# Performance work log

Measured on AMD Instinct MI355X. Metric: run time of the kernel, lower is better.

## Reference

```python
import jax, jax.numpy as jnp
import numpy as np

N, E = 50000, 800000
IN, HID, OUT, H = 128, 32, 32, 4
NEG_SLOPE = 0.2
EPS = 1e-5


def layernorm(x, g, b):
    mu = x.mean(-1, keepdims=True)
    var = ((x - mu) ** 2).mean(-1, keepdims=True)
    return (x - mu) * jax.lax.rsqrt(var + EPS) * g + b


def gat_conv(x, src, dst, W, a_s, a_d, bias, heads, ch, concat):
    n = x.shape[0]
    h = (x @ W).reshape(n, heads, ch)               # [N,H,C]
    alpha_s = (h * a_s).sum(-1)                     # [N,H]
    alpha_d = (h * a_d).sum(-1)                     # [N,H]
    e = jax.nn.leaky_relu(alpha_s[src] + alpha_d[dst], NEG_SLOPE)  # [E,H]
    m = jax.ops.segment_max(e, dst, num_segments=n)
    m = jnp.where(jnp.isfinite(m), m, 0.0)
    ex = jnp.exp(e - m[dst])
    denom = jax.ops.segment_sum(ex, dst, num_segments=n)
    alpha = ex / (denom[dst] + 1e-16)               # [E,H]
    msg = h[src] * alpha[:, :, None]                # [E,H,C]
    out = jax.ops.segment_sum(msg, dst, num_segments=n)  # [N,H,C]
    out = out.reshape(n, heads * ch) if concat else out.mean(axis=1)
    return out + bias


def setup_inputs() -> dict:
    key = jax.random.key(0)
    ks = jax.random.split(key, 24)
    HC = HID * H
    s = 0.05
    inp = {
        "x": jax.random.normal(ks[0], (N, IN), jnp.float32),
        "edge_index": jax.random.randint(ks[1], (2, E), 0, N),
        "W1": jax.random.normal(ks[2], (IN, HC), jnp.float32) * s,
        "as1": jax.random.normal(ks[3], (H, HID), jnp.float32) * s,
        "ad1": jax.random.normal(ks[4], (H, HID), jnp.float32) * s,
        "b1": jnp.zeros((HC,), jnp.float32),
        "g1": jnp.ones((HC,), jnp.float32),
        "be1": jnp.zeros((HC,), jnp.float32),
        "W2": jax.random.normal(ks[5], (HC, HC), jnp.float32) * s,
        "as2": jax.random.normal(ks[6], (H, HID), jnp.float32) * s,
        "ad2": jax.random.normal(ks[7], (H, HID), jnp.float32) * s,
        "b2": jnp.zeros((HC,), jnp.float32),
        "g2": jnp.ones((HC,), jnp.float32),
        "be2": jnp.zeros((HC,), jnp.float32),
        "W3": jax.random.normal(ks[8], (HC, OUT * H), jnp.float32) * s,
        "as3": jax.random.normal(ks[9], (H, OUT), jnp.float32) * s,
        "ad3": jax.random.normal(ks[10], (H, OUT), jnp.float32) * s,
        "b3": jnp.zeros((OUT,), jnp.float32),
        "Wsk": jax.random.normal(ks[11], (IN, HC), jnp.float32) * s,
        "bsk": jnp.zeros((HC,), jnp.float32),
    }
    return inp


def reference(x, edge_index, W1, as1, ad1, b1, g1, be1, W2, as2, ad2, b2, g2, be2, W3, as3, ad3, b3, Wsk, bsk):
    n = x.shape[0]
    loops = jnp.arange(n, dtype=edge_index.dtype)
    src = jnp.concatenate([edge_index[0], loops])
    dst = jnp.concatenate([edge_index[1], loops])
    h = gat_conv(x, src, dst, W1, as1, ad1, b1, H, HID, True)
    h = jax.nn.elu(h)
    h = layernorm(h, g1, be1)
    h = h + (x @ Wsk + bsk)  # residual (dropout is identity in eval)
    h = gat_conv(h, src, dst, W2, as2, ad2, b2, H, HID, True)
    h = jax.nn.elu(h)
    h = layernorm(h, g2, be2)
    h = gat_conv(h, src, dst, W3, as3, ad3, b3, H, OUT, False)
    return h
```

## Files before the change

### kernel.cpp

```cpp
#include <hip/hip_runtime.h>
#include <hip/hip_bf16.h>

typedef __attribute__((ext_vector_type(8))) short short8;
typedef __attribute__((ext_vector_type(4))) float f32x4;
using bf16 = __hip_bfloat16;

#define NEG_SLOPE 0.2f
#define LN_EPS 1e-5f
#define SCAT_EPB 4096

__device__ __forceinline__ unsigned short f2bfu(float v) {
    bf16 t = __float2bfloat16(v);
    unsigned short s;
    __builtin_memcpy(&s, &t, 2);
    return s;
}
__device__ __forceinline__ short f2bf(float v) {
    bf16 t = __float2bfloat16(v);
    short s;
    __builtin_memcpy(&s, &t, 2);
    return s;
}
__device__ __forceinline__ unsigned packbf(float a, float b) {
    return (unsigned)f2bfu(a) | ((unsigned)f2bfu(b) << 16);
}
__device__ __forceinline__ float bflo(unsigned u) { return __uint_as_float(u << 16); }
__device__ __forceinline__ float bfhi(unsigned u) { return __uint_as_float(u & 0xffff0000u); }
__device__ __forceinline__ float bf1(unsigned short u) { return __uint_as_float(((unsigned)u) << 16); }

__device__ __forceinline__ int computeFlag(const void* x) {
    const uint4* u4 = (const uint4*)x;
    int lane = threadIdx.x & 63;
    float m = 0.f;
    for (int i = lane; i < 1024; i += 64) {
        uint4 q = u4[i];
        unsigned vv[4] = {q.x, q.y, q.z, q.w};
#pragma unroll
        for (int k = 0; k < 4; ++k) {
            float a = fabsf(bflo(vv[k]));
            float b = fabsf(bfhi(vv[k]));
            m = fmaxf(m, (a == a) ? a : 1e30f);
            m = fmaxf(m, (b == b) ? b : 1e30f);
        }
    }
    for (int d = 1; d < 64; d <<= 1) m = fmaxf(m, __shfl_xor(m, d));
    return (m > 1e4f) ? 1 : 0;
}

struct Ptr4 { const void* p[4]; };
struct Ptr14 { const void* p[14]; };
struct Ptr3 { const void* p[3]; };
struct Ptr6 { const void* p[6]; };
__global__ void stage_k(const void* __restrict__ x,
                        Ptr4 Ws, bf16* __restrict__ WT,
                        Ptr14 ptrs, bf16* __restrict__ sv,
                        Ptr3 Wv, Ptr6 av, bf16* __restrict__ vaT,
                        int* __restrict__ dtFlag, int* __restrict__ bucketCur,
                        int CAP) {
    int b = blockIdx.x;
    int f = computeFlag(x);
    if (b < 256) {
        int gid = b * 256 + threadIdx.x;
        int m = gid >> 14;
        int idx = gid & 16383;
        int i = idx >> 7, j = idx & 127;
        const void* W = Ws.p[m];
        float v = f ? ((const float*)W)[idx]
                    : __bfloat162float(((const bf16*)W)[idx]);
        WT[m * 16384 + j * 128 + i] = __float2bfloat16(v);
    } else if (b == 256) {
        for (int i = threadIdx.x; i < 512; i += 256) bucketCur[i] = i * CAP;
        if (threadIdx.x == 0) dtFlag[0] = f;
        for (int k = threadIdx.x; k < 14 * 128; k += 256) {
            int t = k >> 7, i = k & 127;
            int n = (t == 12) ? 32 : 128;
            if (i < n) {
                const void* s = ptrs.p[t];
                float v = f ? ((const float*)s)[i]
                            : __bfloat162float(((const bf16*)s)[i]);
                sv[k] = __float2bfloat16(v);
            }
        }
    } else {
        int gid = (b - 257) * 256 + threadIdx.x;
        int l = gid >> 11;
        if (l >= 3) return;
        int c = (gid >> 7) & 15, k = gid & 127;
        float acc = 0.f;
        if (c < 8) {
            int hd = c & 3;
            const void* W = Wv.p[l];
            const void* a = av.p[l * 2 + (c >> 2)];
            for (int j = 0; j < 32; ++j) {
                float wv = f ? ((const float*)W)[k * 128 + hd * 32 + j]
                             : __bfloat162float(((const bf16*)W)[k * 128 + hd * 32 + j]);
                float avv = f ? ((const float*)a)[hd * 32 + j]
                              : __bfloat162float(((const bf16*)a)[hd * 32 + j]);
                acc += wv * avv;
            }
        }
        vaT[gid] = __float2bfloat16(acc);
    }
}

__global__ __launch_bounds__(256) void mega1_k(
        const void* __restrict__ A, const bf16* __restrict__ WT,
        bf16* __restrict__ out0, bf16* __restrict__ out1,
        const bf16* __restrict__ bias1, const bf16* __restrict__ vaT,
        float* __restrict__ asN, float* __restrict__ adN,
        int N, const int* __restrict__ flag, int gb,
        const int* __restrict__ src, const int* __restrict__ dst,
        int* bucketCur, int* __restrict__ ebuf, int E, int NB, int CAP) {
    __shared__ int lcnt[512], lbase[512];
    if ((int)blockIdx.x >= gb) {
        int t = threadIdx.x;
        int e0 = ((int)blockIdx.x - gb) * SCAT_EPB;
        int cnt = E - e0;
        if (cnt > SCAT_EPB) cnt = SCAT_EPB;
        for (int i = t; i < NB; i += 256) lcnt[i] = 0;
        __syncthreads();
        for (int i = t; i < cnt; i += 256)
            atomicAdd(&lcnt[dst[e0 + i] >> 7], 1);
        __syncthreads();
        for (int i = t; i < NB; i += 256) {
            int c = lcnt[i];
            lbase[i] = c ? atomicAdd(&bucketCur[i], c) : 0;
            lcnt[i] = 0;
        }
        __syncthreads();
        for (int i = t; i < cnt; i += 256) {
            int d = dst[e0 + i];
            int b = d >> 7;
            int pos = lbase[b] + atomicAdd(&lcnt[b], 1);
            if (pos < (b + 1) * CAP)
                ebuf[pos] = ((d & 127) << 16) | src[e0 + i];
        }
        return;
    }
    int wave = threadIdx.x >> 6, lane = threadIdx.x & 63;
    int lm = lane & 15, lk = lane >> 4;
    const short* Ws = (const short*)WT;
    const short* Vs = (const short*)vaT;
    bool f32m = flag[0] != 0;

    short8 bw0[2][4], bw1[2][4];
#pragma unroll
    for (int ct = 0; ct < 2; ++ct) {
        int c = (wave * 2 + ct) * 16 + lm;
#pragma unroll
        for (int kk = 0; kk < 4; ++kk) {
            bw0[ct][kk] = *(const short8*)(Ws + (size_t)c * 128 + kk * 32 + lk * 8);
            bw1[ct][kk] = *(const short8*)(Ws + 16384 + (size_t)c * 128 + kk * 32 + lk * 8);
        }
    }
    short8 va8[4];
    if (wave == 0) {
#pragma unroll
        for (int kk = 0; kk < 4; ++kk)
            va8[kk] = *(const short8*)(Vs + (size_t)lm * 128 + kk * 32 + lk * 8);
    }
    float bv[2][4];
#pragma unroll
    for (int ct = 0; ct < 2; ++ct) {
        int c0 = (wave * 2 + ct) * 16 + lk * 4;
#pragma unroll
        for (int i = 0; i < 4; ++i)
            bv[ct][i] = __bfloat162float(bias1[c0 + i]);
    }

    int stride = gb * 32;
    for (int rowBase = blockIdx.x * 32; rowBase < N; rowBase += stride) {
        short8 af[2][4];
#pragma unroll
        for (int rt = 0; rt < 2; ++rt) {
            int r = rowBase + rt * 16 + lm;
            if (r >= N) r = N - 1;
            if (f32m) {
#pragma unroll
                for (int kk = 0; kk < 4; ++kk) {
                    const float* Af = (const float*)A + (size_t)r * 128 + kk * 32 + lk * 8;
                    float4 q0 = *(const float4*)(Af);
                    float4 q1 = *(const float4*)(Af + 4);
                    short8 v;
                    v[0] = f2bf(q0.x); v[1] = f2bf(q0.y); v[2] = f2bf(q0.z); v[3] = f2bf(q0.w);
                    v[4] = f2bf(q1.x); v[5] = f2bf(q1.y); v[6] = f2bf(q1.z); v[7] = f2bf(q1.w);
                    af[rt][kk] = v;
                }
            } else {
#pragma unroll
                for (int kk = 0; kk < 4; ++kk)
                    af[rt][kk] = *(const short8*)((const short*)A + (size_t)r * 128 + kk * 32 + lk * 8);
            }
        }

        f32x4 acc0[2][2], acc1[2][2];
#pragma unroll
        for (int ct = 0; ct < 2; ++ct)
#pragma unroll
            for (int rt = 0; rt < 2; ++rt) {
                acc0[ct][rt] = (f32x4){0.f, 0.f, 0.f, 0.f};
                acc1[ct][rt] = (f32x4){0.f, 0.f, 0.f, 0.f};
            }
#pragma unroll
        for (int rt = 0; rt < 2; ++rt) {
#pragma unroll
            for (int kk = 0; kk < 4; ++kk) {
                acc0[0][rt] = __builtin_amdgcn_mfma_f32_16x16x32_bf16(bw0[0][kk], af[rt][kk], acc0[0][rt], 0, 0, 0);
                acc0[1][rt] = __builtin_amdgcn_mfma_f32_16x16x32_bf16(bw0[1][kk], af[rt][kk], acc0[1][rt], 0, 0, 0);
                acc1[0][rt] = __builtin_amdgcn_mfma_f32_16x16x32_bf16(bw1[0][kk], af[rt][kk], acc1[0][rt], 0, 0, 0);
                acc1[1][rt] = __builtin_amdgcn_mfma_f32_16x16x32_bf16(bw1[1][kk], af[rt][kk], acc1[1][rt], 0, 0, 0);
            }
        }
#pragma unroll
        for (int ct = 0; ct < 2; ++ct) {
            int c0 = (wave * 2 + ct) * 16 + lk * 4;
#pragma unroll
            for (int rt = 0; rt < 2; ++rt) {
                int r = rowBase + rt * 16 + lm;
                if (r < N) {
                    uint2 pk0, pk1;
                    pk0.x = packbf(acc0[ct][rt][0], acc0[ct][rt][1]);
                    pk0.y = packbf(acc0[ct][rt][2], acc0[ct][rt][3]);
                    pk1.x = packbf(acc1[ct][rt][0] + bv[ct][0], acc1[ct][rt][1] + bv[ct][1]);
                    pk1.y = packbf(acc1[ct][rt][2] + bv[ct][2], acc1[ct][rt][3] + bv[ct][3]);
                    *(uint2*)((unsigned short*)out0 + (size_t)r * 128 + c0) = pk0;
                    *(uint2*)((unsigned short*)out1 + (size_t)r * 128 + c0) = pk1;
                }
            }
        }
        if (wave == 0) {
            f32x4 accA[2];
#pragma unroll
            for (int rt = 0; rt < 2; ++rt) accA[rt] = (f32x4){0.f, 0.f, 0.f, 0.f};
#pragma unroll
            for (int rt = 0; rt < 2; ++rt)
#pragma unroll
                for (int kk = 0; kk < 4; ++kk)
                    accA[rt] = __builtin_amdgcn_mfma_f32_16x16x32_bf16(va8[kk], af[rt][kk], accA[rt], 0, 0, 0);
            if (lk < 2) {
                float* dp = lk ? adN : asN;
#pragma unroll
                for (int rt = 0; rt < 2; ++rt) {
                    int r = rowBase + rt * 16 + lm;
                    if (r < N) *(f32x4*)(dp + (size_t)r * 4) = accA[rt];
                }
            }
        }
    }
}

__global__ __launch_bounds__(256) void build_k(const int* __restrict__ ebuf,
                                               const int* __restrict__ bucketCur,
                                               int* __restrict__ rowSE,
                                               int* __restrict__ colSrc,
                                               int N, int CAP) {
    int b = blockIdx.x, t = threadIdx.x;
    int base = b * CAP;
    int cnt = bucketCur[b] - base;
    if (cnt > CAP) cnt = CAP;
    __shared__ int nodeCnt[128], nodeCur[128], ws2[2];
    if (t < 128) nodeCnt[t] = 0;
    __syncthreads();
    for (int i = t; i < cnt; i += 256)
        atomicAdd(&nodeCnt[ebuf[base + i] >> 16], 1);
    __syncthreads();
    int v = 0, incl = 0;
    if (t < 128) {
        v = nodeCnt[t];
        incl = v;
        for (int d = 1; d < 64; d <<= 1) {
            int u = __shfl_up(incl, d);
            if ((t & 63) >= d) incl += u;
        }
        if ((t & 63) == 63) ws2[t >> 6] = incl;
    }
    __syncthreads();
    if (t < 128) {
        int excl = incl - v + ((t >= 64) ? ws2[0] : 0);
        int node = b * 128 + t;
        if (node < N) {
            rowSE[node * 2] = base + excl;
            rowSE[node * 2 + 1] = base + excl + v;
        }
        nodeCur[t] = excl;
    }
    __syncthreads();
    for (int i = t; i < cnt; i += 256) {
        int p = ebuf[base + i];
        int pos = base + atomicAdd(&nodeCur[p >> 16], 1);
        colSrc[pos] = (p & 0xffff) << 8;
    }
}

__global__ __launch_bounds__(256) void gemm_k(const void* __restrict__ A,
                                              const bf16* __restrict__ WT,
                                              bf16* __restrict__ out0,
                                              const bf16* __restrict__ vaT,
                                              float* __restrict__ asN,
                                              float* __restrict__ adN,
                                              int N) {
    int wave = threadIdx.x >> 6, lane = threadIdx.x & 63;
    int lm = lane & 15, lk = lane >> 4;
    const short* Ws = (const short*)WT;
    const short* Vs = (const short*)vaT;

    short8 bw0[2][4];
#pragma unroll
    for (int ct = 0; ct < 2; ++ct) {
        int c = (wave * 2 + ct) * 16 + lm;
#pragma unroll
        for (int kk = 0; kk < 4; ++kk)
            bw0[ct][kk] = *(const short8*)(Ws + (size_t)c * 128 + kk * 32 + lk * 8);
    }
    short8 va8[4];
    if (wave == 0) {
#pragma unroll
        for (int kk = 0; kk < 4; ++kk)
            va8[kk] = *(const short8*)(Vs + (size_t)lm * 128 + kk * 32 + lk * 8);
    }

    int stride = gridDim.x * 32;
    for (int rowBase = blockIdx.x * 32; rowBase < N; rowBase += stride) {
        short8 af[2][4];
#pragma unroll
        for (int rt = 0; rt < 2; ++rt) {
            int r = rowBase + rt * 16 + lm;
            if (r >= N) r = N - 1;
#pragma unroll
            for (int kk = 0; kk < 4; ++kk)
                af[rt][kk] = *(const short8*)((const short*)A + (size_t)r * 128 + kk * 32 + lk * 8);
        }

        f32x4 acc0[2][2];
#pragma unroll
        for (int ct = 0; ct < 2; ++ct)
#pragma unroll
            for (int rt = 0; rt < 2; ++rt) acc0[ct][rt] = (f32x4){0.f, 0.f, 0.f, 0.f};
#pragma unroll
        for (int rt = 0; rt < 2; ++rt) {
#pragma unroll
            for (int kk = 0; kk < 4; ++kk) {
                acc0[0][rt] = __builtin_amdgcn_mfma_f32_16x16x32_bf16(bw0[0][kk], af[rt][kk], acc0[0][rt], 0, 0, 0);
                acc0[1][rt] = __builtin_amdgcn_mfma_f32_16x16x32_bf16(bw0[1][kk], af[rt][kk], acc0[1][rt], 0, 0, 0);
            }
        }
#pragma unroll
        for (int ct = 0; ct < 2; ++ct) {
            int c0 = (wave * 2 + ct) * 16 + lk * 4;
#pragma unroll
            for (int rt = 0; rt < 2; ++rt) {
                int r = rowBase + rt * 16 + lm;
                if (r < N) {
                    uint2 pk;
                    pk.x = packbf(acc0[ct][rt][0], acc0[ct][rt][1]);
                    pk.y = packbf(acc0[ct][rt][2], acc0[ct][rt][3]);
                    *(uint2*)((unsigned short*)out0 + (size_t)r * 128 + c0) = pk;
                }
            }
        }
        if (wave == 0) {
            f32x4 accA[2];
#pragma unroll
            for (int rt = 0; rt < 2; ++rt) accA[rt] = (f32x4){0.f, 0.f, 0.f, 0.f};
#pragma unroll
            for (int rt = 0; rt < 2; ++rt)
#pragma unroll
                for (int kk = 0; kk < 4; ++kk)
                    accA[rt] = __builtin_amdgcn_mfma_f32_16x16x32_bf16(va8[kk], af[rt][kk], accA[rt], 0, 0, 0);
            if (lk < 2) {
                float* dp = lk ? adN : asN;
#pragma unroll
                for (int rt = 0; rt < 2; ++rt) {
                    int r = rowBase + rt * 16 + lm;
                    if (r < N) *(f32x4*)(dp + (size_t)r * 4) = accA[rt];
                }
            }
        }
    }
}

template <int MODE>
__global__ __launch_bounds__(256) void agg_k(const bf16* __restrict__ h,
                                             const float* __restrict__ asN,
                                             const float* __restrict__ adN,
                                             const int* __restrict__ rowSE,
                                             const int* __restrict__ colSrc,
                                             const bf16* __restrict__ bvec,
                                             const bf16* __restrict__ g,
                                             const bf16* __restrict__ be,
                                             void* outv, int N,
                                             const int* __restrict__ flag) {
    int wv = threadIdx.x >> 6, lane = threadIdx.x & 63;
    int grp = lane >> 4, t = lane & 15;
    int hd = t >> 2;
    const char* hbase = (const char*)h + t * 16;
    const char* abase = (const char*)asN + hd * 4;
    int f = (MODE == 3 && flag) ? flag[0] : 0;
    int nstride = gridDim.x * 4;

    for (int n = blockIdx.x * 4 + wv; n < N; n += nstride) {
        int2 se = ((const int2*)rowSE)[n];
        int st = se.x, en = se.y;
        if (en < st) en = st;

        float adn = adN[(size_t)n * 4 + hd];
        float asn_self = asN[(size_t)n * 4 + hd];
        unsigned hs = *(const unsigned*)((const char*)h + (size_t)n * 256 + t * 16 + grp * 4);

        float a[8];
#pragma unroll
        for (int k = 0; k < 8; ++k) a[k] = 0.f;
        float den = 0.f;

        int j = st + grp;
        int o0 = (j      < en) ? colSrc[j]      : 0;
        int o1 = (j + 4  < en) ? colSrc[j + 4]  : 0;
        int o2 = (j + 8  < en) ? colSrc[j + 8]  : 0;
        int o3 = (j + 12 < en) ? colSrc[j + 12] : 0;
        float av0 = *(const float*)(abase + (o0 >> 4));
        uint4 hq0 = *(const uint4*)(hbase + o0);
        float av1 = *(const float*)(abase + (o1 >> 4));
        uint4 hq1 = *(const uint4*)(hbase + o1);
        float av2 = *(const float*)(abase + (o2 >> 4));
        uint4 hq2 = *(const uint4*)(hbase + o2);
        for (; j < en; j += 4) {
            int o4 = (j + 16 < en) ? colSrc[j + 16] : 0;
            float av3 = *(const float*)(abase + (o3 >> 4));
            uint4 hq3 = *(const uint4*)(hbase + o3);
            float e = av0 + adn;
            float w = __expf(fmaxf(e, NEG_SLOPE * e));
            den += w;
            a[0] += w * bflo(hq0.x); a[1] += w * bfhi(hq0.x);
            a[2] += w * bflo(hq0.y); a[3] += w * bfhi(hq0.y);
            a[4] += w * bflo(hq0.z); a[5] += w * bfhi(hq0.z);
            a[6] += w * bflo(hq0.w); a[7] += w * bfhi(hq0.w);
            o3 = o4;
            av0 = av1; hq0 = hq1;
            av1 = av2; hq1 = hq2;
            av2 = av3; hq2 = hq3;
        }

#pragma unroll
        for (int k = 0; k < 8; ++k) {
            a[k] += __shfl_xor(a[k], 16);
            a[k] += __shfl_xor(a[k], 32);
        }
        den += __shfl_xor(den, 16);
        den += __shfl_xor(den, 32);

        float es = asn_self + adn;
        float wsf = __expf(fmaxf(es, NEG_SLOPE * es));
        den += wsf;

        float s0 = (grp & 1) ? a[2] : a[0];
        float s1 = (grp & 1) ? a[3] : a[1];
        float s2 = (grp & 1) ? a[6] : a[4];
        float s3 = (grp & 1) ? a[7] : a[5];
        float p0 = (grp & 2) ? s2 : s0;
        float p1 = (grp & 2) ? s3 : s1;

        p0 += wsf * bflo(hs);
        p1 += wsf * bfhi(hs);

        float inv = 1.f / (den + 1e-16f);
        float y0 = p0 * inv, y1 = p1 * inv;

        if (MODE == 3) {
            y0 += __shfl_xor(y0, 4); y0 += __shfl_xor(y0, 8); y0 *= 0.25f;
            y1 += __shfl_xor(y1, 4); y1 += __shfl_xor(y1, 8); y1 *= 0.25f;
            if (t < 4) {
                int oc = t * 8 + grp * 2;
                unsigned bp = *(const unsigned*)((const char*)bvec + oc * 2);
                float v0 = y0 + bflo(bp), v1 = y1 + bfhi(bp);
                if (f) {
                    *(float2*)((float*)outv + (size_t)n * 32 + oc) = make_float2(v0, v1);
                } else {
                    ((unsigned*)outv)[(size_t)n * 16 + (oc >> 1)] = packbf(v0, v1);
                }
            }
        } else {
            unsigned short* out = (unsigned short*)outv;
            int boff = t * 16 + grp * 4;
            unsigned bp = *(const unsigned*)((const char*)bvec + boff);
            y0 += bflo(bp); y1 += bfhi(bp);
            y0 = y0 > 0.f ? y0 : (__expf(y0) - 1.f);
            y1 = y1 > 0.f ? y1 : (__expf(y1) - 1.f);
            float s = y0 + y1, q = y0 * y0 + y1 * y1;
#pragma unroll
            for (int d = 1; d < 64; d <<= 1) {
                s += __shfl_xor(s, d);
                q += __shfl_xor(q, d);
            }
            float mu = s * (1.f / 128.f);
            float var = q * (1.f / 128.f) - mu * mu;
            var = fmaxf(var, 0.f);
            float rs = rsqrtf(var + LN_EPS);
            unsigned gp = *(const unsigned*)((const char*)g + boff);
            unsigned ep = *(const unsigned*)((const char*)be + boff);
            float z0 = (y0 - mu) * rs * bflo(gp) + bflo(ep);
            float z1 = (y1 - mu) * rs * bfhi(gp) + bfhi(ep);
            char* op = (char*)out + (size_t)n * 256 + boff;
            if (MODE == 1) {
                unsigned sk = *(const unsigned*)op;
                z0 += bflo(sk); z1 += bfhi(sk);
            }
            *(unsigned*)op = packbf(z0, z1);
        }
    }
}

extern "C" void kernel_launch(void* const* d_in, const int* in_sizes, int n_in,
                              void* d_out, int out_size, void* d_ws, size_t ws_size,
                              hipStream_t stream) {
    const void* x  = d_in[0];
    const int*  ei = (const int*)d_in[1];

    int N = in_sizes[0] / 128;
    int E = in_sizes[1] / 2;
    const int* srcI = ei;
    const int* dstI = ei + E;

    int NB = (N + 127) >> 7;
    int CAP = (E / NB + 1024 + 511) & ~511;

    char* w = (char*)d_ws;
    size_t o = 0;
    auto carve = [&](size_t bytes) {
        void* p = w + o;
        o += (bytes + 255) & ~(size_t)255;
        return p;
    };
    int*  dtFlag = (int*)carve(256);
    bf16* WTall = (bf16*)carve(4 * 16384 * 2);
    bf16* sv   = (bf16*)carve(14 * 128 * 2);
    bf16* vaT  = (bf16*)carve(3 * 16 * 128 * 2);
    bf16* hB   = (bf16*)carve((size_t)N * 128 * 2);
    bf16* xB   = (bf16*)carve((size_t)N * 128 * 2);
    float* asN = (float*)carve((size_t)N * 4 * 4);
    float* adN = (float*)carve((size_t)N * 4 * 4);
    int* rowSE = (int*)carve((size_t)N * 2 * 4);
    int* colSrc= (int*)carve((size_t)NB * CAP * 4 + 128);
    int* ebuf  = (int*)carve((size_t)NB * CAP * 4);
    int* bucketCur = (int*)carve(512 * 4);

    Ptr4 wp;
    wp.p[0] = d_in[2];  wp.p[1] = d_in[18];
    wp.p[2] = d_in[8];  wp.p[3] = d_in[14];
    Ptr14 ptrs;
    ptrs.p[0] = d_in[3];  ptrs.p[1] = d_in[4];  ptrs.p[2] = d_in[5];
    ptrs.p[3] = d_in[6];  ptrs.p[4] = d_in[7];
    ptrs.p[5] = d_in[9];  ptrs.p[6] = d_in[10]; ptrs.p[7] = d_in[11];
    ptrs.p[8] = d_in[12]; ptrs.p[9] = d_in[13];
    ptrs.p[10] = d_in[15]; ptrs.p[11] = d_in[16]; ptrs.p[12] = d_in[17];
    ptrs.p[13] = d_in[19];
    Ptr3 wv3;
    wv3.p[0] = d_in[2]; wv3.p[1] = d_in[8]; wv3.p[2] = d_in[14];
    Ptr6 av6;
    av6.p[0] = d_in[3];  av6.p[1] = d_in[4];
    av6.p[2] = d_in[9];  av6.p[3] = d_in[10];
    av6.p[4] = d_in[15]; av6.p[5] = d_in[16];

    stage_k<<<281, 256, 0, stream>>>(x, wp, WTall, ptrs, sv, wv3, av6, vaT,
                                     dtFlag, bucketCur, CAP);

    int gb = (N + 63) / 64;
    int scatB = (E + SCAT_EPB - 1) / SCAT_EPB;
    int nQuads = (N + 3) / 4;
    int aggGrid = nQuads < 2048 ? nQuads : 2048;

    mega1_k<<<gb + scatB, 256, 0, stream>>>(x, WTall, hB, xB, sv + 13 * 128,
                                            vaT, asN, adN, N, dtFlag, gb,
                                            srcI, dstI, bucketCur, ebuf, E, NB, CAP);

    build_k<<<NB, 256, 0, stream>>>(ebuf, bucketCur, rowSE, colSrc, N, CAP);

    agg_k<1><<<aggGrid, 256, 0, stream>>>(hB, asN, adN, rowSE, colSrc,
                                          sv + 2 * 128, sv + 3 * 128, sv + 4 * 128,
                                          xB, N, dtFlag);

    gemm_k<<<gb, 256, 0, stream>>>(xB, WTall + 2 * 16384, hB,
                                   vaT + 2048, asN, adN, N);
    agg_k<2><<<aggGrid, 256, 0, stream>>>(hB, asN, adN, rowSE, colSrc,
                                          sv + 7 * 128, sv + 8 * 128, sv + 9 * 128,
                                          xB, N, dtFlag);

    gemm_k<<<gb, 256, 0, stream>>>(xB, WTall + 3 * 16384, hB,
                                   vaT + 4096, asN, adN, N);
    agg_k<3><<<aggGrid, 256, 0, stream>>>(hB, asN, adN, rowSE, colSrc,
                                          sv + 12 * 128, nullptr, nullptr,
                                          d_out, N, dtFlag);
}
```

Before: 308.0 us.

## Split fused scatter+GEMM megakernel into separate scatter and GEMM kernels

The combined kernel, which ran edge bucket scattering and the first-layer GEMM as different block roles, is split into a dedicated bscatter_k and gemm1_k launched back to back. The scatter chunk size is halved so more blocks share the edge work. This removes the register and LDS pressure that the GEMM path imposed on scatter blocks, and the reverse, at the cost of one extra kernel launch and losing the overlap of the two workloads within one grid.

```diff
diff --git a/kernel.cpp b/kernel.cpp
--- a/kernel.cpp
+++ b/kernel.cpp
@@ -7,7 +7,7 @@
 
 #define NEG_SLOPE 0.2f
 #define LN_EPS 1e-5f
-#define SCAT_EPB 4096
+#define SCAT_EPB 2048
 
 __device__ __forceinline__ unsigned short f2bfu(float v) {
     bf16 t = __float2bfloat16(v);
@@ -26,7 +26,6 @@
 }
 __device__ __forceinline__ float bflo(unsigned u) { return __uint_as_float(u << 16); }
 __device__ __forceinline__ float bfhi(unsigned u) { return __uint_as_float(u & 0xffff0000u); }
-__device__ __forceinline__ float bf1(unsigned short u) { return __uint_as_float(((unsigned)u) << 16); }
 
 __device__ __forceinline__ int computeFlag(const void* x) {
     const uint4* u4 = (const uint4*)x;
@@ -103,40 +102,88 @@
     }
 }
 
-__global__ __launch_bounds__(256) void mega1_k(
-        const void* __restrict__ A, const bf16* __restrict__ WT,
-        bf16* __restrict__ out0, bf16* __restrict__ out1,
-        const bf16* __restrict__ bias1, const bf16* __restrict__ vaT,
-        float* __restrict__ asN, float* __restrict__ adN,
-        int N, const int* __restrict__ flag, int gb,
-        const int* __restrict__ src, const int* __restrict__ dst,
-        int* bucketCur, int* __restrict__ ebuf, int E, int NB, int CAP) {
+__global__ __launch_bounds__(256) void bscatter_k(const int* __restrict__ src,
+                                                  const int* __restrict__ dst,
+                                                  int* bucketCur,
+                                                  int* __restrict__ ebuf,
+                                                  int E, int NB, int CAP) {
     __shared__ int lcnt[512], lbase[512];
-    if ((int)blockIdx.x >= gb) {
-        int t = threadIdx.x;
-        int e0 = ((int)blockIdx.x - gb) * SCAT_EPB;
-        int cnt = E - e0;
-        if (cnt > SCAT_EPB) cnt = SCAT_EPB;
-        for (int i = t; i < NB; i += 256) lcnt[i] = 0;
-        __syncthreads();
-        for (int i = t; i < cnt; i += 256)
-            atomicAdd(&lcnt[dst[e0 + i] >> 7], 1);
-        __syncthreads();
-        for (int i = t; i < NB; i += 256) {
-            int c = lcnt[i];
-            lbase[i] = c ? atomicAdd(&bucketCur[i], c) : 0;
-            lcnt[i] = 0;
-        }
-        __syncthreads();
-        for (int i = t; i < cnt; i += 256) {
-            int d = dst[e0 + i];
-            int b = d >> 7;
-            int pos = lbase[b] + atomicAdd(&lcnt[b], 1);
-            if (pos < (b + 1) * CAP)
-                ebuf[pos] = ((d & 127) << 16) | src[e0 + i];
-        }
-        return;
-    }
+    int t = threadIdx.x;
+    int e0 = blockIdx.x * SCAT_EPB;
+    int cnt = E - e0;
+    if (cnt > SCAT_EPB) cnt = SCAT_EPB;
+    for (int i = t; i < NB; i += 256) lcnt[i] = 0;
+    __syncthreads();
+    for (int i = t; i < cnt; i += 256)
+        atomicAdd(&lcnt[dst[e0 + i] >> 7], 1);
+    __syncthreads();
+    for (int i = t; i < NB; i += 256) {
+        int c = lcnt[i];
+        lbase[i] = c ? atomicAdd(&bucketCur[i], c) : 0;
+        lcnt[i] = 0;
+    }
+    __syncthreads();
+    for (int i = t; i < cnt; i += 256) {
+        int d = dst[e0 + i];
+        int b = d >> 7;
+        int pos = lbase[b] + atomicAdd(&lcnt[b], 1);
+        if (pos < (b + 1) * CAP)
+            ebuf[pos] = ((d & 127) << 16) | src[e0 + i];
+    }
+}
+
+__global__ __launch_bounds__(256) void build_k(const int* __restrict__ ebuf,
+                                               const int* __restrict__ bucketCur,
+                                               int* __restrict__ rowSE,
+                                               int* __restrict__ colSrc,
+                                               int N, int CAP) {
+    int b = blockIdx.x, t = threadIdx.x;
+    int base = b * CAP;
+    int cnt = bucketCur[b] - base;
+    if (cnt > CAP) cnt = CAP;
+    __shared__ int nodeCnt[128], nodeCur[128], ws2[2];
+    if (t < 128) nodeCnt[t] = 0;
+    __syncthreads();
+    for (int i = t; i < cnt; i += 256)
+        atomicAdd(&nodeCnt[ebuf[base + i] >> 16], 1);
+    __syncthreads();
+    int v = 0, incl = 0;
+    if (t < 128) {
+        v = nodeCnt[t];
+        incl = v;
+        for (int d = 1; d < 64; d <<= 1) {
+            int u = __shfl_up(incl, d);
+            if ((t & 63) >= d) incl += u;
+        }
+        if ((t & 63) == 63) ws2[t >> 6] = incl;
+    }
+    __syncthreads();
+    if (t < 128) {
+        int excl = incl - v + ((t >= 64) ? ws2[0] : 0);
+        int node = b * 128 + t;
+        if (node < N) {
+            rowSE[node * 2] = base + excl;
+            rowSE[node * 2 + 1] = base + excl + v;
+        }
+        nodeCur[t] = excl;
+    }
+    __syncthreads();
+    for (int i = t; i < cnt; i += 256) {
+        int p = ebuf[base + i];
+        int pos = base + atomicAdd(&nodeCur[p >> 16], 1);
+        colSrc[pos] = (p & 0xffff) << 8;
+    }
+}
+
+__global__ __launch_bounds__(256) void gemm1_k(const void* __restrict__ A,
+                                               const bf16* __restrict__ WT,
+                                               bf16* __restrict__ out0,
+                                               bf16* __restrict__ out1,
+                                               const bf16* __restrict__ bias1,
+                                               const bf16* __restrict__ vaT,
+                                               float* __restrict__ asN,
+                                               float* __restrict__ adN,
+                                               int N, const int* __restrict__ flag) {
     int wave = threadIdx.x >> 6, lane = threadIdx.x & 63;
     int lm = lane & 15, lk = lane >> 4;
     const short* Ws = (const short*)WT;
@@ -168,7 +215,7 @@
             bv[ct][i] = __bfloat162float(bias1[c0 + i]);
     }
 
-    int stride = gb * 32;
+    int stride = gridDim.x * 32;
     for (int rowBase = blockIdx.x * 32; rowBase < N; rowBase += stride) {
         short8 af[2][4];
 #pragma unroll
@@ -246,49 +293,6 @@
                 }
             }
         }
-    }
-}
-
-__global__ __launch_bounds__(256) void build_k(const int* __restrict__ ebuf,
-                                               const int* __restrict__ bucketCur,
-                                               int* __restrict__ rowSE,
-                                               int* __restrict__ colSrc,
-                                               int N, int CAP) {
-    int b = blockIdx.x, t = threadIdx.x;
-    int base = b * CAP;
-    int cnt = bucketCur[b] - base;
-    if (cnt > CAP) cnt = CAP;
-    __shared__ int nodeCnt[128], nodeCur[128], ws2[2];
-    if (t < 128) nodeCnt[t] = 0;
-    __syncthreads();
-    for (int i = t; i < cnt; i += 256)
-        atomicAdd(&nodeCnt[ebuf[base + i] >> 16], 1);
-    __syncthreads();
-    int v = 0, incl = 0;
-    if (t < 128) {
-        v = nodeCnt[t];
-        incl = v;
-        for (int d = 1; d < 64; d <<= 1) {
-            int u = __shfl_up(incl, d);
-            if ((t & 63) >= d) incl += u;
-        }
-        if ((t & 63) == 63) ws2[t >> 6] = incl;
-    }
-    __syncthreads();
-    if (t < 128) {
-        int excl = incl - v + ((t >= 64) ? ws2[0] : 0);
-        int node = b * 128 + t;
-        if (node < N) {
-            rowSE[node * 2] = base + excl;
-            rowSE[node * 2 + 1] = base + excl + v;
-        }
-        nodeCur[t] = excl;
-    }
-    __syncthreads();
-    for (int i = t; i < cnt; i += 256) {
-        int p = ebuf[base + i];
-        int pos = base + atomicAdd(&nodeCur[p >> 16], 1);
-        colSrc[pos] = (p & 0xffff) << 8;
     }
 }
 
@@ -564,13 +568,14 @@
                                      dtFlag, bucketCur, CAP);
 
     int gb = (N + 63) / 64;
-    int scatB = (E + SCAT_EPB - 1) / SCAT_EPB;
     int nQuads = (N + 3) / 4;
     int aggGrid = nQuads < 2048 ? nQuads : 2048;
 
-    mega1_k<<<gb + scatB, 256, 0, stream>>>(x, WTall, hB, xB, sv + 13 * 128,
-                                            vaT, asN, adN, N, dtFlag, gb,
-                                            srcI, dstI, bucketCur, ebuf, E, NB, CAP);
+    bscatter_k<<<(E + SCAT_EPB - 1) / SCAT_EPB, 256, 0, stream>>>(srcI, dstI,
+                                                                  bucketCur, ebuf, E, NB, CAP);
+
+    gemm1_k<<<gb, 256, 0, stream>>>(x, WTall, hB, xB, sv + 13 * 128,
+                                    vaT, asN, adN, N, dtFlag);
 
     build_k<<<NB, 256, 0, stream>>>(ebuf, bucketCur, rowSE, colSrc, N, CAP);
 
```

Result: slower. 314.6 us (+2.1%).
